# Kernel optimization log

Hardware: AMD Instinct MI355X
Metric: run time of the kernel (lower is better)

Reference implementation:

```python
import jax, jax.numpy as jnp
import numpy as np

K0, K1 = 7, 7          # kernel_size
HEADS, HSIZE = 8, 16   # head_count, head_size
FILTERS = HEADS * HSIZE  # 128
PAD0, PAD1 = K0 // 2, K1 // 2


def unfold_same(x):
    # x: [B,H,W,C] -> patches [B,H,W,C,K0*K1], zero 'SAME' padding, stride 1,
    # kernel positions row-major (matches torch-style C-major unfold after the
    # reshape [B,-1,heads,head_size,kernel_dim] in the original layer).
    B, H, W, C = x.shape
    xp = jnp.pad(x, ((0, 0), (PAD0, PAD0), (PAD1, PAD1), (0, 0)))
    patches = jnp.stack(
        [xp[:, i:i + H, j:j + W, :] for i in range(K0) for j in range(K1)],
        axis=-1)  # [B,H,W,C,K]
    return patches


def setup_inputs() -> dict:
    key = jax.random.key(0)
    ks = jax.random.split(key, 10)
    C = 128
    s = 1.0 / np.sqrt(C)
    inp = {
        "x":   jax.random.normal(ks[0], (4, 64, 64, C), jnp.float32),
        "Wq":  jax.random.normal(ks[1], (C, FILTERS), jnp.float32) * s,
        "bq":  jnp.zeros((FILTERS,), jnp.float32),
        "Wk":  jax.random.normal(ks[2], (C, FILTERS), jnp.float32) * s,
        "bk":  jnp.zeros((FILTERS,), jnp.float32),
        "Wv":  jax.random.normal(ks[3], (C, FILTERS), jnp.float32) * s,
        "bv":  jnp.zeros((FILTERS,), jnp.float32),
        # relative position embeddings: dim0 -> (filters//2, K0, 1), dim1 -> (filters//2, 1, K1)
        "emb0": jax.random.normal(ks[4], (FILTERS // 2, K0, 1), jnp.float32),
        "emb1": jax.random.normal(ks[5], (FILTERS // 2, 1, K1), jnp.float32),
    }
    return inp


def reference(x, Wq, bq, Wk, bk, Wv, bv, emb0, emb1):
    B, H, W, C = x.shape
    KD = K0 * K1

    # 1x1 conv projections
    q = x @ Wq + bq                      # [B,H,W,F]
    k = x @ Wk + bk
    v = x @ Wv + bv

    # queries_unfold has kernel 1, stride 1 -> identity
    q = q.reshape(B, H, W, HEADS, HSIZE)                 # [B,H,W,h,d]

    k_unf = unfold_same(k).reshape(B, H, W, HEADS, HSIZE, KD)  # [B,H,W,h,d,K]
    v_unf = unfold_same(v).reshape(B, H, W, HEADS, HSIZE, KD)

    # relative position embeddings: tile per axis, concat along channel, add to keys
    e0 = jnp.tile(emb0, (1, 1, K1))      # [F/2, K0, K1]
    e1 = jnp.tile(emb1, (1, K0, 1))      # [F/2, K0, K1]
    emb = jnp.concatenate([e0, e1], axis=0).reshape(HEADS, HSIZE, KD)
    k_unf = k_unf + emb                  # broadcast over B,H,W

    # per-pixel attention: scores [B,H,W,h,K] (no sqrt(d) scaling in original)
    scores = jnp.einsum('bxyhd,bxyhdk->bxyhk', q, k_unf)
    attn = jax.nn.softmax(scores, axis=-1)
    out = jnp.einsum('bxyhdk,bxyhk->bxyhd', v_unf, attn)
    return out.reshape(B, H, W, FILTERS)
```

## Files before the change

kernel.cpp:

```cpp
#include <hip/hip_runtime.h>
#include <hip/hip_bf16.h>


constexpr int BB = 4;
constexpr int HH = 64;
constexpr int WW = 64;
constexpr int C  = 128;
constexpr int F  = 128;
constexpr int NPIX = BB * HH * WW;

__device__ __forceinline__ void do_proj(const float* __restrict__ W,
                                        const float* __restrict__ bias,
                                        float* __restrict__ outp,
                                        const float* __restrict__ xs,
                                        int p0, int tp, int tc)
{
    float acc[4][8];
#pragma unroll
    for (int i = 0; i < 4; ++i)
#pragma unroll
        for (int j = 0; j < 8; ++j) acc[i][j] = 0.f;

#pragma unroll 4
    for (int c = 0; c < 128; ++c) {
        const float4 w0 = *(const float4*)(W + c * 128 + tc * 8);
        const float4 w1 = *(const float4*)(W + c * 128 + tc * 8 + 4);
        const float wv[8] = {w0.x, w0.y, w0.z, w0.w, w1.x, w1.y, w1.z, w1.w};
        float xv[4];
#pragma unroll
        for (int i = 0; i < 4; ++i) xv[i] = xs[c * 65 + tp * 4 + i];
#pragma unroll
        for (int i = 0; i < 4; ++i)
#pragma unroll
            for (int j = 0; j < 8; ++j) acc[i][j] = fmaf(xv[i], wv[j], acc[i][j]);
    }

    float bv[8];
#pragma unroll
    for (int j = 0; j < 8; ++j) bv[j] = bias[tc * 8 + j];

#pragma unroll
    for (int i = 0; i < 4; ++i) {
        float4 o0, o1;
        o0.x = acc[i][0] + bv[0];
        o0.y = acc[i][1] + bv[1];
        o0.z = acc[i][2] + bv[2];
        o0.w = acc[i][3] + bv[3];
        o1.x = acc[i][4] + bv[4];
        o1.y = acc[i][5] + bv[5];
        o1.z = acc[i][6] + bv[6];
        o1.w = acc[i][7] + bv[7];
        float* dst = outp + (size_t)(p0 + tp * 4 + i) * F + tc * 8;
        *(float4*)(dst)     = o0;
        *(float4*)(dst + 4) = o1;
    }
}

__global__ __launch_bounds__(256) void proj_kernel(
    const float* __restrict__ x,
    const float* __restrict__ Wq, const float* __restrict__ bq,
    const float* __restrict__ Wk, const float* __restrict__ bk,
    const float* __restrict__ Wv, const float* __restrict__ bv,
    float* __restrict__ qo, float* __restrict__ ko, float* __restrict__ vo)
{
    __shared__ float xs[128 * 65];
    const int t    = threadIdx.x;
    const int g    = blockIdx.x % 3;
    const int tile = blockIdx.x / 3;
    const int p0   = tile * 64;

    for (int idx = t; idx < 64 * 128; idx += 256) {
        const int p = idx >> 7;
        const int c = idx & 127;
        xs[c * 65 + p] = x[(size_t)p0 * C + idx];
    }
    __syncthreads();

    const float* W; const float* bias; float* outp;
    if (g == 0)      { W = Wq; bias = bq; outp = qo; }
    else if (g == 1) { W = Wk; bias = bk; outp = ko; }
    else             { W = Wv; bias = bv; outp = vo; }

    do_proj(W, bias, outp, xs, p0, t >> 4, t & 15);
}

__global__ __launch_bounds__(256, 2) void attn_kernel(
    const float* __restrict__ q, const float* __restrict__ k,
    const float* __restrict__ v, const float* __restrict__ emb0,
    const float* __restrict__ emb1, float* __restrict__ out)
{
    const int t   = threadIdx.x;
    const int pl  = t >> 3;
    const int h   = t & 7;
    const int pix = blockIdx.x * 32 + pl;
    const int xr  = (pix >> 6) & 63;
    const int yc  = pix & 63;

    const float* qp = q + (size_t)pix * F + h * 16;
    float qv[16];
    *(float4*)(&qv[0])  = ((const float4*)qp)[0];
    *(float4*)(&qv[4])  = ((const float4*)qp)[1];
    *(float4*)(&qv[8])  = ((const float4*)qp)[2];
    *(float4*)(&qv[12]) = ((const float4*)qp)[3];

    const float* E = (h < 4) ? (emb0 + h * 16 * 7) : (emb1 + (h - 4) * 16 * 7);
    float qe[7] = {0.f, 0.f, 0.f, 0.f, 0.f, 0.f, 0.f};
#pragma unroll
    for (int d = 0; d < 16; ++d) {
#pragma unroll
        for (int a = 0; a < 7; ++a)
            qe[a] = fmaf(qv[d], E[d * 7 + a], qe[a]);
    }

    float m = -1e30f, l = 0.f;
    float o[16];
#pragma unroll
    for (int d = 0; d < 16; ++d) o[d] = 0.f;

#pragma unroll
    for (int i = 0; i < 7; ++i) {
        const int  xi    = xr + i - 3;
        const bool rowin = ((unsigned)xi < 64u);
        const int  npb   = pix + (i - 3) * 64 - 3;

        float s[7];
#pragma unroll
        for (int j = 0; j < 7; ++j) {
            const int  yj  = yc + j - 3;
            const bool inb = rowin && ((unsigned)yj < 64u);
            int np = npb + j;
            np = min(max(np, 0), NPIX - 1);
            const float* kp = k + (size_t)np * F + h * 16;
            float kb[16];
            *(float4*)(&kb[0])  = ((const float4*)kp)[0];
            *(float4*)(&kb[4])  = ((const float4*)kp)[1];
            *(float4*)(&kb[8])  = ((const float4*)kp)[2];
            *(float4*)(&kb[12]) = ((const float4*)kp)[3];
            float d0 = 0.f, d1 = 0.f, d2 = 0.f, d3 = 0.f;
#pragma unroll
            for (int d = 0; d < 4; ++d) {
                d0 = fmaf(qv[d],      kb[d],      d0);
                d1 = fmaf(qv[4 + d],  kb[4 + d],  d1);
                d2 = fmaf(qv[8 + d],  kb[8 + d],  d2);
                d3 = fmaf(qv[12 + d], kb[12 + d], d3);
            }
            const float dot = (d0 + d1) + (d2 + d3);
            s[j] = (inb ? dot : 0.f) + ((h < 4) ? qe[i] : qe[j]);
        }

        const float rm = fmaxf(fmaxf(fmaxf(s[0], s[1]), fmaxf(s[2], s[3])),
                               fmaxf(fmaxf(s[4], s[5]), s[6]));
        const float mn  = fmaxf(m, rm);
        const float cor = __expf(m - mn);
        float p[7];
#pragma unroll
        for (int j = 0; j < 7; ++j) p[j] = __expf(s[j] - mn);
        l = l * cor + (((p[0] + p[1]) + (p[2] + p[3])) + ((p[4] + p[5]) + p[6]));
        m = mn;
#pragma unroll
        for (int d = 0; d < 16; ++d) o[d] *= cor;

#pragma unroll
        for (int j = 0; j < 7; ++j) {
            const int  yj  = yc + j - 3;
            const bool inb = rowin && ((unsigned)yj < 64u);
            int np = npb + j;
            np = min(max(np, 0), NPIX - 1);
            const float* vp = v + (size_t)np * F + h * 16;
            float vb[16];
            *(float4*)(&vb[0])  = ((const float4*)vp)[0];
            *(float4*)(&vb[4])  = ((const float4*)vp)[1];
            *(float4*)(&vb[8])  = ((const float4*)vp)[2];
            *(float4*)(&vb[12]) = ((const float4*)vp)[3];
            const float pj = inb ? p[j] : 0.f;
#pragma unroll
            for (int d = 0; d < 16; ++d) o[d] = fmaf(pj, vb[d], o[d]);
        }
    }

    const float inv = 1.f / l;
    float* op = out + (size_t)pix * F + h * 16;
    float ov[16];
#pragma unroll
    for (int d = 0; d < 16; ++d) ov[d] = o[d] * inv;
    ((float4*)op)[0] = *(float4*)(&ov[0]);
    ((float4*)op)[1] = *(float4*)(&ov[4]);
    ((float4*)op)[2] = *(float4*)(&ov[8]);
    ((float4*)op)[3] = *(float4*)(&ov[12]);
}

extern "C" void kernel_launch(void* const* d_in, const int* in_sizes, int n_in,
                              void* d_out, int out_size, void* d_ws, size_t ws_size,
                              hipStream_t stream)
{
    const float* x    = (const float*)d_in[0];
    const float* Wq   = (const float*)d_in[1];
    const float* bq   = (const float*)d_in[2];
    const float* Wk   = (const float*)d_in[3];
    const float* bk   = (const float*)d_in[4];
    const float* Wv   = (const float*)d_in[5];
    const float* bv   = (const float*)d_in[6];
    const float* emb0 = (const float*)d_in[7];
    const float* emb1 = (const float*)d_in[8];
    float* out = (float*)d_out;

    float* qb = (float*)d_ws;
    float* kb = qb + (size_t)NPIX * F;
    float* vb = kb + (size_t)NPIX * F;

    proj_kernel<<<(NPIX / 64) * 3, 256, 0, stream>>>(x, Wq, bq, Wk, bk, Wv, bv, qb, kb, vb);
    attn_kernel<<<NPIX / 32, 256, 0, stream>>>(qb, kb, vb, emb0, emb1, out);
}
```

Before: 164.2 us.

## Batch K/V row loads, swizzle block order, and retune launch bounds

In the attention kernel, all seven K vectors and all seven V vectors of each window row are now loaded into register arrays up front, so their memory latency overlaps instead of being serialized per neighbour. Both kernels remap block indices with an XCD-style swizzle (stride 8) to change which tiles run together, for better L2 locality across the chiplets. Launch bounds change to 1 block/SM minimum for attention, freeing more registers for the larger buffers, and 3 for the projection, whose inner loop is unrolled further. The cost is much higher register pressure in the attention kernel, which may lower occupancy.

```diff
diff --git a/kernel.cpp b/kernel.cpp
--- a/kernel.cpp
+++ b/kernel.cpp
@@ -21,7 +21,7 @@
 #pragma unroll
         for (int j = 0; j < 8; ++j) acc[i][j] = 0.f;
 
-#pragma unroll 4
+#pragma unroll 8
     for (int c = 0; c < 128; ++c) {
         const float4 w0 = *(const float4*)(W + c * 128 + tc * 8);
         const float4 w1 = *(const float4*)(W + c * 128 + tc * 8 + 4);
@@ -56,7 +56,7 @@
     }
 }
 
-__global__ __launch_bounds__(256) void proj_kernel(
+__global__ __launch_bounds__(256, 3) void proj_kernel(
     const float* __restrict__ x,
     const float* __restrict__ Wq, const float* __restrict__ bq,
     const float* __restrict__ Wk, const float* __restrict__ bk,
@@ -64,9 +64,11 @@
     float* __restrict__ qo, float* __restrict__ ko, float* __restrict__ vo)
 {
     __shared__ float xs[128 * 65];
-    const int t    = threadIdx.x;
-    const int g    = blockIdx.x % 3;
-    const int tile = blockIdx.x / 3;
+    const int t   = threadIdx.x;
+    const int bid = blockIdx.x;
+    const int swz = (bid & 7) * 96 + (bid >> 3);
+    const int g    = swz % 3;
+    const int tile = swz / 3;
     const int p0   = tile * 64;
 
     for (int idx = t; idx < 64 * 128; idx += 256) {
@@ -84,15 +86,18 @@
     do_proj(W, bias, outp, xs, p0, t >> 4, t & 15);
 }
 
-__global__ __launch_bounds__(256, 2) void attn_kernel(
+__global__ __launch_bounds__(256, 1) void attn_kernel(
     const float* __restrict__ q, const float* __restrict__ k,
     const float* __restrict__ v, const float* __restrict__ emb0,
     const float* __restrict__ emb1, float* __restrict__ out)
 {
+    const int bid = blockIdx.x;
+    const int swz = (bid & 7) * 64 + (bid >> 3);
+
     const int t   = threadIdx.x;
     const int pl  = t >> 3;
     const int h   = t & 7;
-    const int pix = blockIdx.x * 32 + pl;
+    const int pix = swz * 32 + pl;
     const int xr  = (pix >> 6) & 63;
     const int yc  = pix & 63;
 
@@ -123,29 +128,43 @@
         const bool rowin = ((unsigned)xi < 64u);
         const int  npb   = pix + (i - 3) * 64 - 3;
 
+        float kb[7][16];
+#pragma unroll
+        for (int j = 0; j < 7; ++j) {
+            int np = min(max(npb + j, 0), NPIX - 1);
+            const float4* kp = (const float4*)(k + (size_t)np * F + h * 16);
+            *(float4*)(&kb[j][0])  = kp[0];
+            *(float4*)(&kb[j][4])  = kp[1];
+            *(float4*)(&kb[j][8])  = kp[2];
+            *(float4*)(&kb[j][12]) = kp[3];
+        }
+
         float s[7];
 #pragma unroll
         for (int j = 0; j < 7; ++j) {
             const int  yj  = yc + j - 3;
             const bool inb = rowin && ((unsigned)yj < 64u);
-            int np = npb + j;
-            np = min(max(np, 0), NPIX - 1);
-            const float* kp = k + (size_t)np * F + h * 16;
-            float kb[16];
-            *(float4*)(&kb[0])  = ((const float4*)kp)[0];
-            *(float4*)(&kb[4])  = ((const float4*)kp)[1];
-            *(float4*)(&kb[8])  = ((const float4*)kp)[2];
-            *(float4*)(&kb[12]) = ((const float4*)kp)[3];
             float d0 = 0.f, d1 = 0.f, d2 = 0.f, d3 = 0.f;
 #pragma unroll
             for (int d = 0; d < 4; ++d) {
-                d0 = fmaf(qv[d],      kb[d],      d0);
-                d1 = fmaf(qv[4 + d],  kb[4 + d],  d1);
-                d2 = fmaf(qv[8 + d],  kb[8 + d],  d2);
-                d3 = fmaf(qv[12 + d], kb[12 + d], d3);
+                d0 = fmaf(qv[d],      kb[j][d],      d0);
+                d1 = fmaf(qv[4 + d],  kb[j][4 + d],  d1);
+                d2 = fmaf(qv[8 + d],  kb[j][8 + d],  d2);
+                d3 = fmaf(qv[12 + d], kb[j][12 + d], d3);
             }
             const float dot = (d0 + d1) + (d2 + d3);
             s[j] = (inb ? dot : 0.f) + ((h < 4) ? qe[i] : qe[j]);
+        }
+
+        float vb[7][16];
+#pragma unroll
+        for (int j = 0; j < 7; ++j) {
+            int np = min(max(npb + j, 0), NPIX - 1);
+            const float4* vp = (const float4*)(v + (size_t)np * F + h * 16);
+            *(float4*)(&vb[j][0])  = vp[0];
+            *(float4*)(&vb[j][4])  = vp[1];
+            *(float4*)(&vb[j][8])  = vp[2];
+            *(float4*)(&vb[j][12]) = vp[3];
         }
 
         const float rm = fmaxf(fmaxf(fmaxf(s[0], s[1]), fmaxf(s[2], s[3])),
@@ -164,17 +183,9 @@
         for (int j = 0; j < 7; ++j) {
             const int  yj  = yc + j - 3;
             const bool inb = rowin && ((unsigned)yj < 64u);
-            int np = npb + j;
-            np = min(max(np, 0), NPIX - 1);
-            const float* vp = v + (size_t)np * F + h * 16;
-            float vb[16];
-            *(float4*)(&vb[0])  = ((const float4*)vp)[0];
-            *(float4*)(&vb[4])  = ((const float4*)vp)[1];
-            *(float4*)(&vb[8])  = ((const float4*)vp)[2];
-            *(float4*)(&vb[12]) = ((const float4*)vp)[3];
             const float pj = inb ? p[j] : 0.f;
 #pragma unroll
-            for (int d = 0; d < 16; ++d) o[d] = fmaf(pj, vb[d], o[d]);
+            for (int d = 0; d < 16; ++d) o[d] = fmaf(pj, vb[j][d], o[d]);
         }
     }
 
```

After: 159.4 us. 1.03x faster.
